# Kernel tuning notes

Hardware: AMD Instinct MI355X
Metric: run time of the kernel (lower is better)

The kernel has to match this reference:

```python
import jax, jax.numpy as jnp
import numpy as np

VOCAB = 32000
EMBED = 1024
BATCH = 16384
SEQ = 7


def _convolute(X, kernel):
    # X: (B, L, E); kernel: (h, E) -> (B, L-h+1, E)
    h = kernel.shape[0]
    L = X.shape[1]
    out = X[:, 0:L - h + 1] * kernel[0]
    for t in range(1, h):
        out = out + X[:, t:L - h + 1 + t] * kernel[t]
    return out


def setup_inputs() -> dict:
    key = jax.random.key(0)
    k1, k2, k3, k4, k5, k6 = jax.random.split(key, 6)
    X = jax.random.randint(k1, (BATCH, SEQ), 0, VOCAB)
    emb = jax.random.normal(k2, (VOCAB, EMBED), dtype=jnp.float32)
    conv1 = jax.random.normal(k3, (2, EMBED), dtype=jnp.float32)
    conv2 = jax.random.normal(k4, (2, EMBED), dtype=jnp.float32)
    conv3 = jax.random.normal(k5, (3, EMBED), dtype=jnp.float32)
    conv4 = jax.random.normal(k6, (3, EMBED), dtype=jnp.float32)
    return {"X": X, "emb": emb, "conv1": conv1, "conv2": conv2,
            "conv3": conv3, "conv4": conv4}


def reference(X, emb, conv1, conv2, conv3, conv4):
    H = emb[X]                                  # (B, 7, E)
    H = jax.nn.sigmoid(_convolute(H, conv1))    # (B, 6, E)
    H = jax.nn.sigmoid(_convolute(H, conv2))    # (B, 5, E)
    H = jax.nn.sigmoid(_convolute(H, conv3))    # (B, 3, E)
    H = jax.nn.sigmoid(_convolute(H, conv4))    # (B, 1, E)  (scentence_size == 7)
    return H.reshape(H.shape[0], -1)            # (B, E)
```

## Files before the change

kernel.cpp:

```cpp
#include <hip/hip_runtime.h>


constexpr int EMBED = 1024;
constexpr int SEQ   = 7;
constexpr int ROWS  = 8;
constexpr int TAPS  = 10;

typedef float f2 __attribute__((ext_vector_type(2)));
typedef float f4 __attribute__((ext_vector_type(4)));

__device__ __forceinline__ f2 sig2(f2 y) {
    f2 u;
    u.x = __builtin_amdgcn_exp2f(y.x);
    u.y = __builtin_amdgcn_exp2f(y.y);
    f2 d = u + (f2){1.0f, 1.0f};
    f2 r;
    r.x = __builtin_amdgcn_rcpf(d.x);
    r.y = __builtin_amdgcn_rcpf(d.y);
    return r;
}

__device__ __forceinline__ void gather_row(const float* __restrict__ emb,
                                           const int idx[SEQ],
                                           int e, f2 v[SEQ][2]) {
#pragma unroll
    for (int t = 0; t < SEQ; ++t) {
        const f4 f = *(const f4*)(emb + (size_t)idx[t] * EMBED + e);
        v[t][0] = (f2){f.x, f.y};
        v[t][1] = (f2){f.z, f.w};
    }
}

__device__ __forceinline__ void ldw(const float* wl, int tap, int e, f2 w[2]) {
    const f4 f = *(const f4*)(wl + tap * EMBED + e);
    w[0] = (f2){f.x, f.y};
    w[1] = (f2){f.z, f.w};
}

__device__ __forceinline__ void compute_row(const f2 v[SEQ][2], const float* wl,
                                            int e, float* __restrict__ outp) {
    f2 wa[2], wb[2], wc[2];

    f2 h1[6][2];
    ldw(wl, 0, e, wa); ldw(wl, 1, e, wb);
#pragma unroll
    for (int l = 0; l < 6; ++l)
#pragma unroll
        for (int p = 0; p < 2; ++p)
            h1[l][p] = sig2(v[l][p] * wa[p] + v[l + 1][p] * wb[p]);

    f2 h2[5][2];
    ldw(wl, 2, e, wa); ldw(wl, 3, e, wb);
#pragma unroll
    for (int l = 0; l < 5; ++l)
#pragma unroll
        for (int p = 0; p < 2; ++p)
            h2[l][p] = sig2(h1[l][p] * wa[p] + h1[l + 1][p] * wb[p]);

    f2 h3[3][2];
    ldw(wl, 4, e, wa); ldw(wl, 5, e, wb); ldw(wl, 6, e, wc);
#pragma unroll
    for (int l = 0; l < 3; ++l)
#pragma unroll
        for (int p = 0; p < 2; ++p)
            h3[l][p] = sig2(h2[l][p] * wa[p] + h2[l + 1][p] * wb[p]
                            + h2[l + 2][p] * wc[p]);

    f2 o[2];
    ldw(wl, 7, e, wa); ldw(wl, 8, e, wb); ldw(wl, 9, e, wc);
#pragma unroll
    for (int p = 0; p < 2; ++p)
        o[p] = sig2(h3[0][p] * wa[p] + h3[1][p] * wb[p] + h3[2][p] * wc[p]);

    f4 of;
    of.x = o[0].x; of.y = o[0].y; of.z = o[1].x; of.w = o[1].y;
    __builtin_nontemporal_store(of, (f4*)outp);
}

__global__ __launch_bounds__(256, 4) void CSM_62216896250023_kernel(
    const int*   __restrict__ X,
    const float* __restrict__ emb,
    const float* __restrict__ c1,
    const float* __restrict__ c2,
    const float* __restrict__ c3,
    const float* __restrict__ c4,
    float*       __restrict__ out)
{
    __shared__ float wlds[TAPS * EMBED];

    const int tid = threadIdx.x;
    const int e   = tid << 2;
    const int b0  = blockIdx.x * ROWS;

    const float NL2E = -1.44269504088896f;
    {
        const float* src[TAPS] = {c1, c1 + EMBED,
                                  c2, c2 + EMBED,
                                  c3, c3 + EMBED, c3 + 2 * EMBED,
                                  c4, c4 + EMBED, c4 + 2 * EMBED};
#pragma unroll
        for (int t = 0; t < TAPS; ++t) {
            f4 f = *(const f4*)(src[t] + e);
            f *= NL2E;
            *(f4*)&wlds[t * EMBED + e] = f;
        }
    }

    int idx[ROWS][SEQ];
#pragma unroll
    for (int r = 0; r < ROWS; ++r)
#pragma unroll
        for (int t = 0; t < SEQ; ++t)
            idx[r][t] = X[(b0 + r) * SEQ + t];

    __syncthreads();

    f2 v[2][SEQ][2];
    gather_row(emb, idx[0], e, v[0]);
#pragma unroll
    for (int r = 0; r < ROWS; ++r) {
        if (r + 1 < ROWS) gather_row(emb, idx[r + 1], e, v[(r + 1) & 1]);
        __builtin_amdgcn_sched_barrier(0);
        unsigned rofs = 0;
        asm volatile("" : "+v"(rofs));
        compute_row(v[r & 1], (const float*)wlds + rofs, e,
                    out + (size_t)(b0 + r) * EMBED + e);
    }
}

extern "C" void kernel_launch(void* const* d_in, const int* in_sizes, int n_in,
                              void* d_out, int out_size, void* d_ws, size_t ws_size,
                              hipStream_t stream) {
    const int*   X   = (const int*)d_in[0];
    const float* emb = (const float*)d_in[1];
    const float* c1  = (const float*)d_in[2];
    const float* c2  = (const float*)d_in[3];
    const float* c3  = (const float*)d_in[4];
    const float* c4  = (const float*)d_in[5];
    float* out = (float*)d_out;

    const int batch = in_sizes[0] / SEQ;
    CSM_62216896250023_kernel<<<batch / ROWS, 256, 0, stream>>>(X, emb, c1, c2, c3, c4, out);
}
```

Before: 276.9 us.

## Hand-schedule embedding gathers with inline asm loads and explicit vmcnt waits

Replaces compiler-generated gather loads with inline-asm global_load_dwordx4 using scalar base plus vector offset (row indices moved to SGPRs via readfirstlane), and inserts explicit s_waitcnt vmcnt so the next row's seven loads stay in flight while the current row computes. Output stores become asm global stores (no longer nontemporal), the compute is reorganized per half-vector to cut live registers, and the occupancy hint in launch_bounds is dropped. The aim is to stop the compiler from waiting on all outstanding loads before compute. The risk is that the hand-written vmcnt counts are wrong, since stores also count toward vmcnt on some targets, and that register pressure rises.

```diff
diff --git a/kernel.cpp b/kernel.cpp
--- a/kernel.cpp
+++ b/kernel.cpp
@@ -20,64 +20,60 @@
     return r;
 }
 
-__device__ __forceinline__ void gather_row(const float* __restrict__ emb,
-                                           const int idx[SEQ],
-                                           int e, f2 v[SEQ][2]) {
+__device__ __forceinline__ f2 vhalf(f4 f, int p) {
+    return p ? (f2){f.z, f.w} : (f2){f.x, f.y};
+}
+
+__device__ __forceinline__ void issue_row_loads(const float* __restrict__ emb,
+                                                const int idx7[SEQ],
+                                                unsigned voff, f4 v[SEQ]) {
 #pragma unroll
     for (int t = 0; t < SEQ; ++t) {
-        const f4 f = *(const f4*)(emb + (size_t)idx[t] * EMBED + e);
-        v[t][0] = (f2){f.x, f.y};
-        v[t][1] = (f2){f.z, f.w};
+        const float* p = emb + ((size_t)(unsigned)idx7[t]) * EMBED;
+        asm volatile("global_load_dwordx4 %0, %1, %2"
+                     : "=v"(v[t])
+                     : "v"(voff), "s"(p));
     }
 }
 
-__device__ __forceinline__ void ldw(const float* wl, int tap, int e, f2 w[2]) {
-    const f4 f = *(const f4*)(wl + tap * EMBED + e);
-    w[0] = (f2){f.x, f.y};
-    w[1] = (f2){f.z, f.w};
+__device__ __forceinline__ void store_row(float* obase, unsigned voff, f4 val) {
+    asm volatile("global_store_dwordx4 %0, %1, %2"
+                 :: "v"(voff), "v"(val), "s"(obase)
+                 : "memory");
 }
 
-__device__ __forceinline__ void compute_row(const f2 v[SEQ][2], const float* wl,
-                                            int e, float* __restrict__ outp) {
-    f2 wa[2], wb[2], wc[2];
+__device__ __forceinline__ f2 ldw2(const float* wl, int tap, int e, int p) {
+    return *(const f2*)(wl + tap * EMBED + e + 2 * p);
+}
 
-    f2 h1[6][2];
-    ldw(wl, 0, e, wa); ldw(wl, 1, e, wb);
+__device__ __forceinline__ f4 compute_row(const f4 v[SEQ], const float* wl, int e) {
+    f2 o[2];
 #pragma unroll
-    for (int l = 0; l < 6; ++l)
+    for (int p = 0; p < 2; ++p) {
+        f2 wa = ldw2(wl, 0, e, p), wb = ldw2(wl, 1, e, p), wc;
+        f2 h1[6];
 #pragma unroll
-        for (int p = 0; p < 2; ++p)
-            h1[l][p] = sig2(v[l][p] * wa[p] + v[l + 1][p] * wb[p]);
-
-    f2 h2[5][2];
-    ldw(wl, 2, e, wa); ldw(wl, 3, e, wb);
+        for (int l = 0; l < 6; ++l)
+            h1[l] = sig2(vhalf(v[l], p) * wa + vhalf(v[l + 1], p) * wb);
+        wa = ldw2(wl, 2, e, p); wb = ldw2(wl, 3, e, p);
+        f2 h2[5];
 #pragma unroll
-    for (int l = 0; l < 5; ++l)
+        for (int l = 0; l < 5; ++l)
+            h2[l] = sig2(h1[l] * wa + h1[l + 1] * wb);
+        wa = ldw2(wl, 4, e, p); wb = ldw2(wl, 5, e, p); wc = ldw2(wl, 6, e, p);
+        f2 h3[3];
 #pragma unroll
-        for (int p = 0; p < 2; ++p)
-            h2[l][p] = sig2(h1[l][p] * wa[p] + h1[l + 1][p] * wb[p]);
-
-    f2 h3[3][2];
-    ldw(wl, 4, e, wa); ldw(wl, 5, e, wb); ldw(wl, 6, e, wc);
-#pragma unroll
-    for (int l = 0; l < 3; ++l)
-#pragma unroll
-        for (int p = 0; p < 2; ++p)
-            h3[l][p] = sig2(h2[l][p] * wa[p] + h2[l + 1][p] * wb[p]
-                            + h2[l + 2][p] * wc[p]);
-
-    f2 o[2];
-    ldw(wl, 7, e, wa); ldw(wl, 8, e, wb); ldw(wl, 9, e, wc);
-#pragma unroll
-    for (int p = 0; p < 2; ++p)
-        o[p] = sig2(h3[0][p] * wa[p] + h3[1][p] * wb[p] + h3[2][p] * wc[p]);
-
+        for (int l = 0; l < 3; ++l)
+            h3[l] = sig2(h2[l] * wa + h2[l + 1] * wb + h2[l + 2] * wc);
+        wa = ldw2(wl, 7, e, p); wb = ldw2(wl, 8, e, p); wc = ldw2(wl, 9, e, p);
+        o[p] = sig2(h3[0] * wa + h3[1] * wb + h3[2] * wc);
+    }
     f4 of;
     of.x = o[0].x; of.y = o[0].y; of.z = o[1].x; of.w = o[1].y;
-    __builtin_nontemporal_store(of, (f4*)outp);
+    return of;
 }
 
-__global__ __launch_bounds__(256, 4) void CSM_62216896250023_kernel(
+__global__ __launch_bounds__(256) void CSM_62216896250023_kernel(
     const int*   __restrict__ X,
     const float* __restrict__ emb,
     const float* __restrict__ c1,
@@ -90,6 +86,7 @@
 
     const int tid = threadIdx.x;
     const int e   = tid << 2;
+    const unsigned voff = (unsigned)e * 4u;
     const int b0  = blockIdx.x * ROWS;
 
     const float NL2E = -1.44269504088896f;
@@ -111,21 +108,32 @@
     for (int r = 0; r < ROWS; ++r)
 #pragma unroll
         for (int t = 0; t < SEQ; ++t)
-            idx[r][t] = X[(b0 + r) * SEQ + t];
+            idx[r][t] = __builtin_amdgcn_readfirstlane(X[(b0 + r) * SEQ + t]);
 
     __syncthreads();
 
-    f2 v[2][SEQ][2];
-    gather_row(emb, idx[0], e, v[0]);
+    f4 va[SEQ], vb[SEQ];
+    issue_row_loads(emb, idx[0], voff, va);
+
 #pragma unroll
     for (int r = 0; r < ROWS; ++r) {
-        if (r + 1 < ROWS) gather_row(emb, idx[r + 1], e, v[(r + 1) & 1]);
+        if (r + 1 < ROWS) {
+            if (r & 1) issue_row_loads(emb, idx[r + 1], voff, va);
+            else       issue_row_loads(emb, idx[r + 1], voff, vb);
+        }
+        if (r == 0)              asm volatile("s_waitcnt vmcnt(7)" ::: "memory");
+        else if (r == ROWS - 1)  asm volatile("s_waitcnt vmcnt(1)" ::: "memory");
+        else                     asm volatile("s_waitcnt vmcnt(8)" ::: "memory");
         __builtin_amdgcn_sched_barrier(0);
+
         unsigned rofs = 0;
         asm volatile("" : "+v"(rofs));
-        compute_row(v[r & 1], (const float*)wlds + rofs, e,
-                    out + (size_t)(b0 + r) * EMBED + e);
+        const float* wl = (const float*)wlds + rofs;
+        f4 o = (r & 1) ? compute_row(vb, wl, e) : compute_row(va, wl, e);
+        store_row(out + (size_t)(b0 + r) * EMBED, voff, o);
     }
+
+    asm volatile("s_waitcnt vmcnt(0)" ::: "memory");
 }
 
 extern "C" void kernel_launch(void* const* d_in, const int* in_sizes, int n_in,
```

New measurement: 247.8 us. 10.5% less time.
